# Kernel optimization log

Measured on AMD Instinct MI355X. Metric: run time of the kernel, lower is better.

The kernel has to match this reference:

```python
import jax, jax.numpy as jnp
import numpy as np
import math

T = 120      # frame_num == audio_len == max_seq_len
D = 64       # hidden_layer_size
H = 2        # n_head
DH = D // H
DFF = 2 * D
DOUT = 31
PERIOD = 10
EPS = 1e-5
NEG = -1e9
SCALE = 1.0 / math.sqrt(DH)
SLOPES = (1.0 / 16.0, 1.0 / 256.0)  # ALiBi slopes for n_head=2


def _pe():
    # PeriodicPositionalEncoding: sinusoid over one period, tiled
    pos = jnp.arange(PERIOD, dtype=jnp.float32)[:, None]
    div = jnp.exp(jnp.arange(0, D, 2, dtype=jnp.float32) * (-math.log(10000.0) / D))
    s, c = jnp.sin(pos * div), jnp.cos(pos * div)
    pe = jnp.stack([s, c], axis=-1).reshape(PERIOD, D)  # interleave sin/cos
    return jnp.tile(pe, (T // PERIOD + 1, 1))[:T]


def _alibi_mask():
    # causal mask + ALiBi bias: alibi[i,j] = -slope * floor((i-j)/period) for j<=i
    slopes = jnp.array(SLOPES, dtype=jnp.float32)
    i = jnp.arange(T)[:, None]
    j = jnp.arange(T)[None, :]
    rel = ((i - j) // PERIOD).astype(jnp.float32)
    return jnp.where(j <= i, -slopes[:, None, None] * rel, NEG)  # [H,T,T]


def _ln(x, g, b):
    m = x.mean(-1, keepdims=True)
    v = ((x - m) ** 2).mean(-1, keepdims=True)
    return (x - m) / jnp.sqrt(v + EPS) * g + b


def setup_inputs() -> dict:
    key = jax.random.key(0)
    ks = iter(jax.random.split(key, 32))
    n = lambda shape, s=0.05: jax.random.normal(next(ks), shape, dtype=jnp.float32) * s
    inp = {
        'audio': jax.random.normal(next(ks), (1, T, 1024), dtype=jnp.float32),
        'W_audio': n((D, 1024)), 'b_audio': n((D,)),
        'obj_W': n((D, 5)),
        'Wq': n((D, D)), 'bq': n((D,)), 'Wk': n((D, D)), 'bk': n((D,)),
        'Wv': n((D, D)), 'bv': n((D,)), 'Wo': n((D, D)), 'bo': n((D,)),
        'Wv2': n((D, D)), 'bv2': n((D,)), 'Wo2': n((D, D)), 'bo2': n((D,)),
        'g1': jnp.ones((D,)), 'be1': jnp.zeros((D,)),
        'g2': jnp.ones((D,)), 'be2': jnp.zeros((D,)),
        'g3': jnp.ones((D,)), 'be3': jnp.zeros((D,)),
        'W1': n((DFF, D)), 'c1': n((DFF,)), 'W2': n((D, DFF)), 'c2': n((D,)),
        'Wr': n((DOUT, D)), 'br': n((DOUT,)), 'Wm': n((D, DOUT)), 'bm': n((D,)),
    }
    return inp


def _forward(audio, W_audio, b_audio, obj_W, Wq, bq, Wk, bk, Wv, bv, Wo, bo,
             Wv2, bv2, Wo2, bo2, g1, be1, g2, be2, g3, be3,
             W1, c1, W2, c2, Wr, br, Wm, bm):
    mem = audio[0] @ W_audio.T + b_audio          # [S,D], S == T
    style = obj_W[:, 0]                            # obj_vector @ [1,0,0,0,0]
    pe = _pe()
    mask = _alibi_mask()
    slopes = jnp.array(SLOPES, dtype=jnp.float32)
    jarr = jnp.arange(T)

    # enc_dec_mask leaves exactly one memory key per target row (anti-diagonal
    # from the end); the feedback row t at step t always attends memory[-1],
    # so its cross-attn output is just the projected value of the last frame.
    cross_last = (mem[-1] @ Wv2.T + bv2) @ Wo2.T + bo2  # [D]

    def step(emb, t):
        # decode only the last row (row t) of the growing sequence; 1-layer
        # post-norm decoder => row t depends only on input rows 0..t.
        x = emb + pe                                 # PPE over prefix
        xq = jnp.take(x, t, axis=0)                  # [D]
        q = (xq @ Wq.T + bq).reshape(H, DH)
        k = (x @ Wk.T + bk).reshape(T, H, DH)
        v = (x @ Wv.T + bv).reshape(T, H, DH)
        bias = jnp.where(jarr <= t,
                         -slopes[:, None] * ((t - jarr) // PERIOD).astype(jnp.float32),
                         NEG)                        # [H,T]
        sc = jnp.einsum('hd,shd->hs', q, k) * SCALE + bias
        a = jax.nn.softmax(sc, axis=-1)
        sa = jnp.einsum('hs,shd->hd', a, v).reshape(D) @ Wo.T + bo
        h1 = _ln(xq + sa, g1, be1)
        h2 = _ln(h1 + cross_last, g2, be2)
        h3 = _ln(h2 + jax.nn.relu(h2 @ W1.T + c1) @ W2.T + c2, g3, be3)
        new = (h3 @ Wr.T + br) @ Wm.T + bm + style   # vertice_map(vertice_map_r(.)) + style
        emb = jax.lax.dynamic_update_slice(emb, new[None, :], (t + 1, 0))
        return emb, None

    emb0 = jnp.zeros((T, D), audio.dtype).at[0].set(style)
    emb, _ = jax.lax.scan(step, emb0, jnp.arange(T - 1))

    # final full-length decode (last loop iteration of the torch module)
    x = emb + pe
    q = (x @ Wq.T + bq).reshape(T, H, DH)
    k = (x @ Wk.T + bk).reshape(T, H, DH)
    v = (x @ Wv.T + bv).reshape(T, H, DH)
    sc = jnp.einsum('thd,shd->hts', q, k) * SCALE + mask
    a = jax.nn.softmax(sc, axis=-1)
    sa = jnp.einsum('hts,shd->thd', a, v).reshape(T, D) @ Wo.T + bo
    h1 = _ln(x + sa, g1, be1)
    # at length T with S == T the enc_dec_mask aligns target row j <-> memory row j
    cross = (mem @ Wv2.T + bv2) @ Wo2.T + bo2
    h2 = _ln(h1 + cross, g2, be2)
    h3 = _ln(h2 + jax.nn.relu(h2 @ W1.T + c1) @ W2.T + c2, g3, be3)
    return (h3 @ Wr.T + br)[None]                    # [1,T,31]


def reference(audio, W_audio, b_audio, obj_W, Wq, bq, Wk, bk, Wv, bv, Wo, bo,
              Wv2, bv2, Wo2, bo2, g1, be1, g2, be2, g3, be3,
              W1, c1, W2, c2, Wr, br, Wm, bm):
    return _forward(audio, W_audio, b_audio, obj_W, Wq, bq, Wk, bk, Wv, bv, Wo, bo,
                    Wv2, bv2, Wo2, bo2, g1, be1, g2, be2, g3, be3,
                    W1, c1, W2, c2, Wr, br, Wm, bm)
```

## Files before the change

kernel.cpp:

```cpp
#include <hip/hip_runtime.h>

typedef unsigned short u16;
typedef unsigned int   u32;
typedef _Float16 f16;
typedef f16 h2 __attribute__((ext_vector_type(2)));
typedef f16 h4 __attribute__((ext_vector_type(4)));
typedef f16 h8 __attribute__((ext_vector_type(8)));

#define T_    120
#define D_    64
#define DOUT_ 31
#define KROW_ 68
#define VROW_ 132

#if defined(__has_builtin)
#if __has_builtin(__builtin_amdgcn_fdot2)
#define DOT2(a,b,c) __builtin_amdgcn_fdot2((a),(b),(c),false)
#endif
#endif
#ifndef DOT2
#define DOT2(a,b,c) ((float)(a).x*(float)(b).x + ((float)(a).y*(float)(b).y + (c)))
#endif
#define SHV(x,i,j) __builtin_shufflevector((x),(x),(i),(j))

__device__ __forceinline__ h2 pk(float a, float b){
#if defined(__has_builtin) && __has_builtin(__builtin_amdgcn_cvt_pkrtz)
  return __builtin_bit_cast(h2, __builtin_amdgcn_cvt_pkrtz(a, b));
#else
  h2 r; r.x = (f16)a; r.y = (f16)b; return r;
#endif
}
__device__ __forceinline__ float b2f(u16 u){ return __uint_as_float(((u32)u) << 16); }
__device__ __forceinline__ float2 bp2(u32 u){
  float2 r; r.x = __uint_as_float(u << 16); r.y = __uint_as_float(u & 0xffff0000u); return r;
}
__device__ __forceinline__ u16 f2bu(float f){
  u32 u = __float_as_uint(f);
  u32 r = u + 0x7fffu + ((u >> 16) & 1u);
  return (u16)(r >> 16);
}
__device__ __forceinline__ u16 f2h16(float x){
  f16 v = (f16)x; u16 r; __builtin_memcpy(&r, &v, 2); return r;
}
#define WSYNC() do{ __asm__ __volatile__("" ::: "memory"); __builtin_amdgcn_wave_barrier(); }while(0)

__device__ __forceinline__ float dpp_sum(float x){
  int t;
  t = __builtin_amdgcn_update_dpp(0, __float_as_int(x), 0x111, 0xf, 0xf, true); x += __int_as_float(t);
  t = __builtin_amdgcn_update_dpp(0, __float_as_int(x), 0x112, 0xf, 0xf, true); x += __int_as_float(t);
  t = __builtin_amdgcn_update_dpp(0, __float_as_int(x), 0x114, 0xf, 0xf, true); x += __int_as_float(t);
  t = __builtin_amdgcn_update_dpp(0, __float_as_int(x), 0x118, 0xf, 0xf, true); x += __int_as_float(t);
  t = __builtin_amdgcn_update_dpp(0, __float_as_int(x), 0x142, 0xf, 0xf, true); x += __int_as_float(t);
  t = __builtin_amdgcn_update_dpp(0, __float_as_int(x), 0x143, 0xf, 0xf, true); x += __int_as_float(t);
  return __int_as_float(__builtin_amdgcn_readlane(__float_as_int(x), 63));
}
__device__ __forceinline__ float dpp_max_pos(float x){
  int t;
  t = __builtin_amdgcn_update_dpp(0, __float_as_int(x), 0x111, 0xf, 0xf, true); x = fmaxf(x, __int_as_float(t));
  t = __builtin_amdgcn_update_dpp(0, __float_as_int(x), 0x112, 0xf, 0xf, true); x = fmaxf(x, __int_as_float(t));
  t = __builtin_amdgcn_update_dpp(0, __float_as_int(x), 0x114, 0xf, 0xf, true); x = fmaxf(x, __int_as_float(t));
  t = __builtin_amdgcn_update_dpp(0, __float_as_int(x), 0x118, 0xf, 0xf, true); x = fmaxf(x, __int_as_float(t));
  t = __builtin_amdgcn_update_dpp(0, __float_as_int(x), 0x142, 0xf, 0xf, true); x = fmaxf(x, __int_as_float(t));
  t = __builtin_amdgcn_update_dpp(0, __float_as_int(x), 0x143, 0xf, 0xf, true); x = fmaxf(x, __int_as_float(t));
  return __int_as_float(__builtin_amdgcn_readlane(__float_as_int(x), 63));
}
__device__ __forceinline__ float pe_val(int row, int i){
  const float coef = -0.28782313662425574f;
  int p = row % 10;
  float dv  = __expf((float)(i >> 1) * coef);
  float ang = (float)p * dv;
  return (i & 1) ? __cosf(ang) : __sinf(ang);
}
__device__ __forceinline__ void loadrow32(h2* dst, const float* row){
  #pragma unroll
  for (int r = 0; r < 16; ++r){
    float4 f = ((const float4*)row)[r];
    dst[2*r]   = pk(f.x, f.y);
    dst[2*r+1] = pk(f.z, f.w);
  }
}

__global__ __launch_bounds__(256) void k_pre(const float* __restrict__ audio,
                                             const float* __restrict__ Wa, const float* __restrict__ ba,
                                             const float* __restrict__ Wv2, const float* __restrict__ bv2,
                                             const float* __restrict__ Wo2, const float* __restrict__ bo2,
                                             const float* __restrict__ Wo, const float* __restrict__ W1,
                                             const float* __restrict__ W2, const float* __restrict__ Wr,
                                             const float* __restrict__ Wm, const float* __restrict__ br,
                                             const float* __restrict__ bm,
                                             float* __restrict__ cross, float* __restrict__ Ms,
                                             float* __restrict__ bMv,
                                             u16* __restrict__ wob, u16* __restrict__ w1b,
                                             u16* __restrict__ w2b, u16* __restrict__ wrb){
  const int b = blockIdx.x, tid = threadIdx.x;
  if (b == 120){
    for (int i = tid; i < 4096; i += 256) wob[i] = f2bu(Wo[i]);
    for (int i = tid; i < 8192; i += 256){ w1b[i] = f2bu(W1[i]); w2b[i] = f2bu(W2[i]); }
    for (int i = tid; i < 1984; i += 256) wrb[i] = f2bu(Wr[i]);
    for (int idx = tid; idx < 4096; idx += 256){
      int d = idx >> 6, e = idx & 63;
      float acc = 0.f;
      #pragma unroll
      for (int j = 0; j < 31; ++j) acc += Wm[d*31 + j] * Wr[j*64 + e];
      Ms[idx] = acc;
    }
    if (tid < 64){
      float acc = bm[tid];
      #pragma unroll
      for (int j = 0; j < 31; ++j) acc += Wm[tid*31 + j] * br[j];
      bMv[tid] = acc;
    }
    return;
  }
  __shared__ float ash[1024];
  __shared__ float msh[64], tsh[64];
  for (int i = tid; i < 1024; i += 256) ash[i] = audio[b*1024 + i];
  __syncthreads();
  const int w = tid >> 6, lane = tid & 63;
  for (int d = w*16; d < w*16 + 16; ++d){
    const float4* row = (const float4*)(Wa + d*1024);
    float acc = 0.f;
    #pragma unroll
    for (int m = 0; m < 4; ++m){
      float4 wp = row[lane + 64*m];
      int j = 4*(lane + 64*m);
      acc += wp.x*ash[j] + wp.y*ash[j+1] + wp.z*ash[j+2] + wp.w*ash[j+3];
    }
    acc = dpp_sum(acc);
    if (lane == 0) msh[d] = acc + ba[d];
  }
  __syncthreads();
  if (tid < 64){
    const float4* r1 = (const float4*)(Wv2 + tid*64);
    float a = bv2[tid];
    #pragma unroll
    for (int j = 0; j < 16; ++j){ float4 p = r1[j]; a += p.x*msh[4*j] + p.y*msh[4*j+1] + p.z*msh[4*j+2] + p.w*msh[4*j+3]; }
    tsh[tid] = a;
  }
  __syncthreads();
  if (tid < 64){
    const float4* r2 = (const float4*)(Wo2 + tid*64);
    float c = bo2[tid];
    #pragma unroll
    for (int j = 0; j < 16; ++j){ float4 p = r2[j]; c += p.x*tsh[4*j] + p.y*tsh[4*j+1] + p.z*tsh[4*j+2] + p.w*tsh[4*j+3]; }
    cross[b*64 + tid] = c;
  }
}

__global__ __launch_bounds__(128, 1) void k_scan(
    const float* __restrict__ objW,
    const float* __restrict__ Wq, const float* __restrict__ bq,
    const float* __restrict__ Wk, const float* __restrict__ bk,
    const float* __restrict__ Wv, const float* __restrict__ bv,
    const float* __restrict__ Wo, const float* __restrict__ bo,
    const float* __restrict__ g1, const float* __restrict__ be1,
    const float* __restrict__ g2, const float* __restrict__ be2,
    const float* __restrict__ g3, const float* __restrict__ be3,
    const float* __restrict__ W1, const float* __restrict__ c1,
    const float* __restrict__ W2, const float* __restrict__ c2,
    const float* __restrict__ Ms, const float* __restrict__ bMv,
    const float* __restrict__ cross,
    u16* __restrict__ xw16, u16* __restrict__ Kw16, u16* __restrict__ Vw16)
{
  __shared__ __align__(16) f16 KcS[128*KROW_];
  __shared__ __align__(16) f16 VcS[D_*VROW_];
  __shared__ __align__(16) f16 xwS[T_*D_];
  __shared__ __align__(16) f16 sch[256];
  __shared__ __align__(16) f16 xh[64], qh[64], ath[64], h2h[64], h3h[64];
  __shared__ __align__(16) f16 fsh[128];
  __shared__ float at_p1[64], h2f[64], xf[64];
  __shared__ float pe_tab[640];

  const int tid = threadIdx.x;
  const int i = tid & 63;
  const bool w0 = tid < 64;

  h2 A[32], B[32], C[32], D[32], E[32];
  float biasA=0.f, biasB=0.f, bo_r=0.f, c1r=0.f, c2_r=0.f, bmst=0.f, cls_r=0.f;
  float g1r=0.f,b1r=0.f,g2r=0.f,b2r=0.f,g3r=0.f,b3r=0.f;

  if (w0){
    loadrow32(A, Wq + i*64);
    loadrow32(B, Wv + i*64);
    loadrow32(C, Wo + i*64);
    loadrow32(D, W1 + i*64);
    biasA = bq[i]; biasB = bv[i]; bo_r = bo[i]; c1r = c1[i];
    g1r = g1[i]; b1r = be1[i]; g2r = g2[i]; b2r = be2[i];
    cls_r = cross[119*64 + i];
  } else {
    loadrow32(A, Wk + i*64);
    loadrow32(B, W1 + (64+i)*64);
    loadrow32(C, W2 + i*128);
    loadrow32(D, W2 + i*128 + 64);
    loadrow32(E, Ms + i*64);
    biasA = bk[i]; c1r = c1[64+i]; c2_r = c2[i];
    g3r = g3[i]; b3r = be3[i];
    bmst = bMv[i] + objW[i*5];
  }
  { u32* p = (u32*)KcS; for (int idx = tid; idx < 128*KROW_/2; idx += 128) p[idx] = 0; }
  { u32* p = (u32*)VcS; for (int idx = tid; idx < D_*VROW_/2;  idx += 128) p[idx] = 0; }
  for (int idx = tid; idx < 640; idx += 128) pe_tab[idx] = pe_val(idx >> 6, idx & 63);
  if (w0){
    float st = objW[i*5];
    float x0 = st + pe_val(0, i);
    xf[i] = x0; xh[i] = (f16)x0; xwS[i] = (f16)x0;
  }
  __syncthreads();

  int pp = 1;
  for (int t = 0; t < T_-1; ++t){
    {
      const h8* xv = (const h8*)xh;
      if (w0){
        float q0=biasA,q1=0.f,q2=0.f,q3=0.f, v0=biasB,v1=0.f,v2=0.f,v3=0.f;
        #pragma unroll
        for (int r = 0; r < 8; ++r){
          h8 x = xv[r];
          h2 xa=SHV(x,0,1), xb=SHV(x,2,3), xc=SHV(x,4,5), xd=SHV(x,6,7);
          q0 = DOT2(A[4*r+0], xa, q0); q1 = DOT2(A[4*r+1], xb, q1);
          q2 = DOT2(A[4*r+2], xc, q2); q3 = DOT2(A[4*r+3], xd, q3);
          v0 = DOT2(B[4*r+0], xa, v0); v1 = DOT2(B[4*r+1], xb, v1);
          v2 = DOT2(B[4*r+2], xc, v2); v3 = DOT2(B[4*r+3], xd, v3);
        }
        qh[i] = (f16)((q0+q1)+(q2+q3));
        VcS[i*VROW_ + t] = (f16)((v0+v1)+(v2+v3));
      } else {
        float k0=biasA,k1=0.f,k2=0.f,k3=0.f;
        #pragma unroll
        for (int r = 0; r < 8; ++r){
          h8 x = xv[r];
          k0 = DOT2(A[4*r+0], SHV(x,0,1), k0);
          k1 = DOT2(A[4*r+1], SHV(x,2,3), k1);
          k2 = DOT2(A[4*r+2], SHV(x,4,5), k2);
          k3 = DOT2(A[4*r+3], SHV(x,6,7), k3);
        }
        KcS[t*KROW_ + i] = (f16)((k0+k1)+(k2+k3));
      }
    }
    __syncthreads();
    {
      const int h = tid >> 6, j = i;
      const h8* qv = (const h8*)(qh + h*32);
      const h4* k0 = (const h4*)(KcS + j*KROW_ + h*32);
      const h4* k1 = (const h4*)(KcS + (j+64)*KROW_ + h*32);
      float d0a=0.f,d0b=0.f,d1a=0.f,d1b=0.f;
      #pragma unroll
      for (int r = 0; r < 4; ++r){
        h8 q = qv[r];
        h4 ka = k0[2*r], kb = k0[2*r+1], kc = k1[2*r], kd = k1[2*r+1];
        d0a = DOT2(SHV(ka,0,1), SHV(q,0,1), d0a);
        d0b = DOT2(SHV(ka,2,3), SHV(q,2,3), d0b);
        d0a = DOT2(SHV(kb,0,1), SHV(q,4,5), d0a);
        d0b = DOT2(SHV(kb,2,3), SHV(q,6,7), d0b);
        d1a = DOT2(SHV(kc,0,1), SHV(q,0,1), d1a);
        d1b = DOT2(SHV(kc,2,3), SHV(q,2,3), d1b);
        d1a = DOT2(SHV(kd,0,1), SHV(q,4,5), d1a);
        d1b = DOT2(SHV(kd,2,3), SHV(q,6,7), d1b);
      }
      float d0 = d0a + d0b, d1 = d1a + d1b;
      const float slope = h ? 0.00390625f : 0.0625f;
      int r0 = (t - j) / 10, r1 = (t - j - 64) / 10;
      float s0 = (j      <= t) ? d0*0.17677669529663687f - slope*(float)r0 : -1e30f;
      float s1 = (j + 64 <= t) ? d1*0.17677669529663687f - slope*(float)r1 : -1e30f;
      float m = dpp_max_pos(fmaxf(s0, s1) + 16384.f) - 16384.f;
      float e0 = (j      <= t) ? __expf(s0 - m) : 0.f;
      float e1 = (j + 64 <= t) ? __expf(s1 - m) : 0.f;
      float inv = 1.f / dpp_sum(e0 + e1);
      sch[h*128 + j]      = (f16)(e0*inv);
      sch[h*128 + j + 64] = (f16)(e1*inv);
    }
    __syncthreads();
    float atp0 = 0.f;
    {
      const int hd = i >> 5;
      const h8* av = (const h8*)(sch + hd*128) + (w0 ? 0 : 8);
      const h4* vv = (const h4*)(VcS + i*VROW_) + (w0 ? 0 : 16);
      float p0=0.f,p1=0.f,p2=0.f,p3=0.f;
      #pragma unroll
      for (int r = 0; r < 8; ++r){
        h8 a = av[r];
        h4 va = vv[2*r], vb = vv[2*r+1];
        p0 = DOT2(SHV(va,0,1), SHV(a,0,1), p0);
        p1 = DOT2(SHV(va,2,3), SHV(a,2,3), p1);
        p2 = DOT2(SHV(vb,0,1), SHV(a,4,5), p2);
        p3 = DOT2(SHV(vb,2,3), SHV(a,6,7), p3);
      }
      float p = (p0+p1)+(p2+p3);
      if (!w0) at_p1[i] = p; else atp0 = p;
    }
    __syncthreads();
    if (w0){
      float atv = atp0 + at_p1[i];
      ath[i] = (f16)atv;
      WSYNC();
      const h8* av = (const h8*)ath;
      float a0=bo_r, a1=0.f, a2=0.f, a3=0.f;
      #pragma unroll
      for (int r = 0; r < 8; ++r){
        h8 x = av[r];
        a0 = DOT2(C[4*r+0], SHV(x,0,1), a0);
        a1 = DOT2(C[4*r+1], SHV(x,2,3), a1);
        a2 = DOT2(C[4*r+2], SHV(x,4,5), a2);
        a3 = DOT2(C[4*r+3], SHV(x,6,7), a3);
      }
      float y = xf[i] + (a0+a1)+(a2+a3);
      float s = dpp_sum(y), s2 = dpp_sum(y*y);
      float m = s*(1.f/64.f), var = fmaxf(s2*(1.f/64.f) - m*m, 0.f);
      float h1 = (y - m)*rsqrtf(var + 1e-5f)*g1r + b1r;
      float z = h1 + cls_r;
      float sz = dpp_sum(z), sz2 = dpp_sum(z*z);
      float mz = sz*(1.f/64.f), vz = fmaxf(sz2*(1.f/64.f) - mz*mz, 0.f);
      float h2v = (z - mz)*rsqrtf(vz + 1e-5f)*g2r + b2r;
      h2h[i] = (f16)h2v;
      h2f[i] = h2v;
    }
    __syncthreads();
    {
      const h8* hv = (const h8*)h2h;
      float a0=c1r, a1=0.f, a2=0.f, a3=0.f;
      if (w0){
        #pragma unroll
        for (int r = 0; r < 8; ++r){
          h8 x = hv[r];
          a0 = DOT2(D[4*r+0], SHV(x,0,1), a0);
          a1 = DOT2(D[4*r+1], SHV(x,2,3), a1);
          a2 = DOT2(D[4*r+2], SHV(x,4,5), a2);
          a3 = DOT2(D[4*r+3], SHV(x,6,7), a3);
        }
      } else {
        #pragma unroll
        for (int r = 0; r < 8; ++r){
          h8 x = hv[r];
          a0 = DOT2(B[4*r+0], SHV(x,0,1), a0);
          a1 = DOT2(B[4*r+1], SHV(x,2,3), a1);
          a2 = DOT2(B[4*r+2], SHV(x,4,5), a2);
          a3 = DOT2(B[4*r+3], SHV(x,6,7), a3);
        }
      }
      fsh[tid] = (f16)fmaxf((a0+a1)+(a2+a3), 0.f);
    }
    __syncthreads();
    if (!w0){
      const h8* fv = (const h8*)fsh;
      float a0=c2_r, a1=0.f, a2=0.f, a3=0.f;
      #pragma unroll
      for (int r = 0; r < 8; ++r){
        h8 x = fv[r];
        a0 = DOT2(C[4*r+0], SHV(x,0,1), a0);
        a1 = DOT2(C[4*r+1], SHV(x,2,3), a1);
        a2 = DOT2(C[4*r+2], SHV(x,4,5), a2);
        a3 = DOT2(C[4*r+3], SHV(x,6,7), a3);
      }
      #pragma unroll
      for (int r = 0; r < 8; ++r){
        h8 x = fv[8+r];
        a0 = DOT2(D[4*r+0], SHV(x,0,1), a0);
        a1 = DOT2(D[4*r+1], SHV(x,2,3), a1);
        a2 = DOT2(D[4*r+2], SHV(x,4,5), a2);
        a3 = DOT2(D[4*r+3], SHV(x,6,7), a3);
      }
      float y = h2f[i] + (a0+a1)+(a2+a3);
      float s = dpp_sum(y), s2 = dpp_sum(y*y);
      float m = s*(1.f/64.f), var = fmaxf(s2*(1.f/64.f) - m*m, 0.f);
      float h3v = (y - m)*rsqrtf(var + 1e-5f)*g3r + b3r;
      h3h[i] = (f16)h3v;
      WSYNC();
      const h8* hv3 = (const h8*)h3h;
      float m0=bmst, m1=0.f, m2=0.f, m3=0.f;
      #pragma unroll
      for (int r = 0; r < 8; ++r){
        h8 x = hv3[r];
        m0 = DOT2(E[4*r+0], SHV(x,0,1), m0);
        m1 = DOT2(E[4*r+1], SHV(x,2,3), m1);
        m2 = DOT2(E[4*r+2], SHV(x,4,5), m2);
        m3 = DOT2(E[4*r+3], SHV(x,6,7), m3);
      }
      float xn = (m0+m1)+(m2+m3) + pe_tab[pp*64 + i];
      xf[i] = xn;
      xh[i] = (f16)xn;
      xwS[(t+1)*64 + i] = (f16)xn;
    }
    __syncthreads();
    pp = (pp == 9) ? 0 : pp + 1;
  }
  {
    const h8* xv = (const h8*)xh;
    if (w0){
      float v0=biasB,v1=0.f,v2=0.f,v3=0.f;
      #pragma unroll
      for (int r = 0; r < 8; ++r){
        h8 x = xv[r];
        v0 = DOT2(B[4*r+0], SHV(x,0,1), v0);
        v1 = DOT2(B[4*r+1], SHV(x,2,3), v1);
        v2 = DOT2(B[4*r+2], SHV(x,4,5), v2);
        v3 = DOT2(B[4*r+3], SHV(x,6,7), v3);
      }
      Vw16[119*64 + i] = f2h16((v0+v1)+(v2+v3));
    } else {
      float k0=biasA,k1=0.f,k2=0.f,k3=0.f;
      #pragma unroll
      for (int r = 0; r < 8; ++r){
        h8 x = xv[r];
        k0 = DOT2(A[4*r+0], SHV(x,0,1), k0);
        k1 = DOT2(A[4*r+1], SHV(x,2,3), k1);
        k2 = DOT2(A[4*r+2], SHV(x,4,5), k2);
        k3 = DOT2(A[4*r+3], SHV(x,6,7), k3);
      }
      Kw16[119*64 + i] = f2h16((k0+k1)+(k2+k3));
    }
  }
  {
    const u16* kc = (const u16*)KcS;
    const u16* vc = (const u16*)VcS;
    for (int idx = tid; idx < 119*64; idx += 128){
      int t_ = idx >> 6, d = idx & 63;
      Kw16[idx] = kc[t_*KROW_ + d];
      Vw16[idx] = vc[d*VROW_ + t_];
    }
    const u32* xs32 = (const u32*)xwS;
    for (int idx = tid; idx < T_*D_/2; idx += 128) ((u32*)xw16)[idx] = xs32[idx];
  }
}

__global__ __launch_bounds__(128) void k_final(
    const float* __restrict__ Wq, const float* __restrict__ bq, const float* __restrict__ bo,
    const float* __restrict__ g1, const float* __restrict__ be1,
    const float* __restrict__ g2, const float* __restrict__ be2,
    const float* __restrict__ g3, const float* __restrict__ be3,
    const float* __restrict__ c1, const float* __restrict__ c2, const float* __restrict__ br,
    const u16* __restrict__ wo_b, const u16* __restrict__ w1_b,
    const u16* __restrict__ w2_b, const u16* __restrict__ wr_b,
    const float* __restrict__ cross, const u16* __restrict__ xw16,
    const u16* __restrict__ Kw16, const u16* __restrict__ Vw16,
    float* __restrict__ out)
{
  __shared__ float xs[64], qs[64], at[64], h2s[64], h3s[64], fs[128], sc[256];
  const int irow = blockIdx.x, tid = threadIdx.x;
  const f16* xp = (const f16*)xw16;
  const f16* kp = (const f16*)Kw16;
  const f16* vp = (const f16*)Vw16;
  if (tid < 64) xs[tid] = (float)xp[irow*64 + tid];
  __syncthreads();
  if (tid < 64){
    const float4* wr_ = (const float4*)(Wq + tid*64);
    float acc = bq[tid];
    #pragma unroll
    for (int j = 0; j < 16; ++j){ float4 w = wr_[j]; acc += w.x*xs[4*j] + w.y*xs[4*j+1] + w.z*xs[4*j+2] + w.w*xs[4*j+3]; }
    qs[tid] = acc;
  }
  __syncthreads();
  {
    const int h = tid >> 6, j = tid & 63;
    const float* qh_ = qs + h*32;
    float d0 = 0.f, d1 = 0.f;
    const h4* k0 = (const h4*)(kp + j*64 + h*32);
    #pragma unroll
    for (int w = 0; w < 8; ++w){
      h4 p = k0[w];
      d0 += (float)p.x*qh_[4*w] + (float)p.y*qh_[4*w+1] + (float)p.z*qh_[4*w+2] + (float)p.w*qh_[4*w+3];
    }
    if (j < 56){
      const h4* k1 = (const h4*)(kp + (j+64)*64 + h*32);
      #pragma unroll
      for (int w = 0; w < 8; ++w){
        h4 p = k1[w];
        d1 += (float)p.x*qh_[4*w] + (float)p.y*qh_[4*w+1] + (float)p.z*qh_[4*w+2] + (float)p.w*qh_[4*w+3];
      }
    }
    const float slope = h ? 0.00390625f : 0.0625f;
    float s0 = (j      <= irow) ? d0*0.17677669529663687f - slope*(float)((irow-j)/10)    : -1e30f;
    float s1 = (j + 64 <= irow) ? d1*0.17677669529663687f - slope*(float)((irow-j-64)/10) : -1e30f;
    float m = dpp_max_pos(fmaxf(s0, s1) + 16384.f) - 16384.f;
    float e0 = (j      <= irow) ? __expf(s0 - m) : 0.f;
    float e1 = (j + 64 <= irow) ? __expf(s1 - m) : 0.f;
    float inv = 1.f / dpp_sum(e0 + e1);
    sc[h*128 + j]      = e0*inv;
    sc[h*128 + j + 64] = e1*inv;
  }
  __syncthreads();
  if (tid < 64){
    const float* a = sc + (tid >> 5)*128;
    float a0=0.f,a1=0.f,a2=0.f,a3=0.f;
    #pragma unroll
    for (int jj = 0; jj < 30; ++jj){
      a0 += a[4*jj]   * (float)vp[(4*jj)*64   + tid];
      a1 += a[4*jj+1] * (float)vp[(4*jj+1)*64 + tid];
      a2 += a[4*jj+2] * (float)vp[(4*jj+2)*64 + tid];
      a3 += a[4*jj+3] * (float)vp[(4*jj+3)*64 + tid];
    }
    at[tid] = (a0+a1)+(a2+a3);
  }
  __syncthreads();
  if (tid < 64){
    const u32* orow = (const u32*)(wo_b + tid*64);
    float acc = bo[tid];
    #pragma unroll
    for (int w = 0; w < 32; ++w){ float2 p = bp2(orow[w]); acc += p.x*at[2*w] + p.y*at[2*w+1]; }
    float y = xs[tid] + acc;
    float s = dpp_sum(y), s2 = dpp_sum(y*y);
    float m = s*(1.f/64.f), var = fmaxf(s2*(1.f/64.f) - m*m, 0.f);
    float h1 = (y - m)*rsqrtf(var + 1e-5f)*g1[tid] + be1[tid];
    float z = h1 + cross[irow*64 + tid];
    float sz = dpp_sum(z), sz2 = dpp_sum(z*z);
    float mz = sz*(1.f/64.f), vz = fmaxf(sz2*(1.f/64.f) - mz*mz, 0.f);
    h2s[tid] = (z - mz)*rsqrtf(vz + 1e-5f)*g2[tid] + be2[tid];
  }
  __syncthreads();
  {
    const u32* w1r = (const u32*)(w1_b + tid*64);
    float acc = c1[tid];
    #pragma unroll
    for (int w = 0; w < 32; ++w){ float2 p = bp2(w1r[w]); acc += p.x*h2s[2*w] + p.y*h2s[2*w+1]; }
    fs[tid] = fmaxf(acc, 0.f);
  }
  __syncthreads();
  if (tid < 64){
    const u32* w2r = (const u32*)(w2_b + tid*128);
    float acc = c2[tid];
    #pragma unroll
    for (int w = 0; w < 64; ++w){ float2 p = bp2(w2r[w]); acc += p.x*fs[2*w] + p.y*fs[2*w+1]; }
    float y = h2s[tid] + acc;
    float s = dpp_sum(y), s2 = dpp_sum(y*y);
    float m = s*(1.f/64.f), var = fmaxf(s2*(1.f/64.f) - m*m, 0.f);
    h3s[tid] = (y - m)*rsqrtf(var + 1e-5f)*g3[tid] + be3[tid];
  }
  __syncthreads();
  if (tid < DOUT_){
    const u32* rr = (const u32*)(wr_b + tid*64);
    float acc = br[tid];
    #pragma unroll
    for (int w = 0; w < 32; ++w){ float2 p = bp2(rr[w]); acc += p.x*h3s[2*w] + p.y*h3s[2*w+1]; }
    out[irow*DOUT_ + tid] = acc;
  }
}

extern "C" void kernel_launch(void* const* d_in, const int* in_sizes, int n_in,
                              void* d_out, int out_size, void* d_ws, size_t ws_size,
                              hipStream_t stream){
  const float* audio=(const float*)d_in[0];
  const float* Wa   =(const float*)d_in[1];
  const float* ba   =(const float*)d_in[2];
  const float* objW =(const float*)d_in[3];
  const float* Wq   =(const float*)d_in[4];
  const float* bq   =(const float*)d_in[5];
  const float* Wk   =(const float*)d_in[6];
  const float* bk   =(const float*)d_in[7];
  const float* Wv   =(const float*)d_in[8];
  const float* bv   =(const float*)d_in[9];
  const float* Wo   =(const float*)d_in[10];
  const float* bo   =(const float*)d_in[11];
  const float* Wv2  =(const float*)d_in[12];
  const float* bv2  =(const float*)d_in[13];
  const float* Wo2  =(const float*)d_in[14];
  const float* bo2  =(const float*)d_in[15];
  const float* g1   =(const float*)d_in[16];
  const float* be1  =(const float*)d_in[17];
  const float* g2   =(const float*)d_in[18];
  const float* be2  =(const float*)d_in[19];
  const float* g3   =(const float*)d_in[20];
  const float* be3  =(const float*)d_in[21];
  const float* W1   =(const float*)d_in[22];
  const float* c1   =(const float*)d_in[23];
  const float* W2   =(const float*)d_in[24];
  const float* c2   =(const float*)d_in[25];
  const float* Wr   =(const float*)d_in[26];
  const float* br   =(const float*)d_in[27];
  const float* Wm   =(const float*)d_in[28];
  const float* bm   =(const float*)d_in[29];

  float* ws    = (float*)d_ws;
  float* cross = ws;
  float* Ms    = ws + 7680;
  float* bMv   = ws + 11776;
  u16* xw16 = (u16*)(ws + 11840);
  u16* Kw16 = xw16 + 7680;
  u16* Vw16 = Kw16 + 7680;
  u16* wo_b = Vw16 + 7680;
  u16* w1_b = wo_b + 4096;
  u16* w2_b = w1_b + 8192;
  u16* wr_b = w2_b + 8192;
  float* out = (float*)d_out;

  k_pre  <<<dim3(121), dim3(256), 0, stream>>>(audio, Wa, ba, Wv2, bv2, Wo2, bo2,
                                               Wo, W1, W2, Wr, Wm, br, bm,
                                               cross, Ms, bMv, wo_b, w1_b, w2_b, wr_b);
  k_scan <<<dim3(1),   dim3(128), 0, stream>>>(objW, Wq, bq, Wk, bk, Wv, bv, Wo, bo,
                                               g1, be1, g2, be2, g3, be3,
                                               W1, c1, W2, c2, Ms, bMv,
                                               cross, xw16, Kw16, Vw16);
  k_final<<<dim3(120), dim3(128), 0, stream>>>(Wq, bq, bo, g1, be1, g2, be2, g3, be3,
                                               c1, c2, br, wo_b, w1_b, w2_b, wr_b,
                                               cross, xw16, Kw16, Vw16, out);
}
```

Before: 393.7 us.

## Defer softmax normalization, fold LN3 into motion projection, rebalance QKV work

The attention softmax drops the max-reduction and instead clamps exponents, applying the 1/sum normalization after the AV and Wo products, so the reduction overlaps with the AV work. LayerNorm3's gain and bias are folded into the Ms projection weights so the LN statistics reduction runs alongside the dot products. The V projection moves after the first barrier so Q/K and V are computed in parallel across both waves, and the second-half AV product is skipped while t<64. Clamping exponents at 8 and skipping the max subtraction risk fp16 overflow or precision drift.

```diff
diff --git a/kernel.cpp b/kernel.cpp
--- a/kernel.cpp
+++ b/kernel.cpp
@@ -41,6 +41,13 @@
 }
 __device__ __forceinline__ u16 f2h16(float x){
   f16 v = (f16)x; u16 r; __builtin_memcpy(&r, &v, 2); return r;
+}
+__device__ __forceinline__ float fast_rcp(float x){
+#if defined(__has_builtin) && __has_builtin(__builtin_amdgcn_rcpf)
+  return __builtin_amdgcn_rcpf(x);
+#else
+  return 1.f / x;
+#endif
 }
 #define WSYNC() do{ __asm__ __volatile__("" ::: "memory"); __builtin_amdgcn_wave_barrier(); }while(0)
 
@@ -166,9 +173,11 @@
   __shared__ __align__(16) f16 VcS[D_*VROW_];
   __shared__ __align__(16) f16 xwS[T_*D_];
   __shared__ __align__(16) f16 sch[256];
-  __shared__ __align__(16) f16 xh[64], qh[64], ath[64], h2h[64], h3h[64];
+  __shared__ __align__(16) f16 xh[64], qh[64], h2h[64], h3h[64];
+  __shared__ __align__(16) f16 at0h[64], at1h[64];
   __shared__ __align__(16) f16 fsh[128];
-  __shared__ float at_p1[64], h2f[64], xf[64];
+  __shared__ float h2f[64], xf[64];
+  __shared__ float invSh;
   __shared__ float pe_tab[640];
 
   const int tid = threadIdx.x;
@@ -176,8 +185,9 @@
   const bool w0 = tid < 64;
 
   h2 A[32], B[32], C[32], D[32], E[32];
-  float biasA=0.f, biasB=0.f, bo_r=0.f, c1r=0.f, c2_r=0.f, bmst=0.f, cls_r=0.f;
-  float g1r=0.f,b1r=0.f,g2r=0.f,b2r=0.f,g3r=0.f,b3r=0.f;
+  float biasA=0.f, biasB=0.f, bo_r=0.f, c1r=0.f, c2_r=0.f, cls_r=0.f;
+  float g1r=0.f,b1r=0.f,g2r=0.f,b2r=0.f;
+  float mg_r=0.f, u_r=0.f;
 
   if (w0){
     loadrow32(A, Wq + i*64);
@@ -192,10 +202,24 @@
     loadrow32(B, W1 + (64+i)*64);
     loadrow32(C, W2 + i*128);
     loadrow32(D, W2 + i*128 + 64);
-    loadrow32(E, Ms + i*64);
+    {
+      const float4* mr  = (const float4*)(Ms + i*64);
+      const float4* gv  = (const float4*)g3;
+      const float4* b3v = (const float4*)be3;
+      float mg = 0.f, mb = 0.f;
+      #pragma unroll
+      for (int r = 0; r < 16; ++r){
+        float4 f = mr[r], g = gv[r], b = b3v[r];
+        float e0 = f.x*g.x, e1 = f.y*g.y, e2 = f.z*g.z, e3 = f.w*g.w;
+        E[2*r]   = pk(e0, e1);
+        E[2*r+1] = pk(e2, e3);
+        mg += (e0+e1)+(e2+e3);
+        mb += f.x*b.x + f.y*b.y + f.z*b.z + f.w*b.w;
+      }
+      mg_r = mg;
+      u_r  = bMv[i] + objW[i*5] + mb;
+    }
     biasA = bk[i]; c1r = c1[64+i]; c2_r = c2[i];
-    g3r = g3[i]; b3r = be3[i];
-    bmst = bMv[i] + objW[i*5];
   }
   { u32* p = (u32*)KcS; for (int idx = tid; idx < 128*KROW_/2; idx += 128) p[idx] = 0; }
   { u32* p = (u32*)VcS; for (int idx = tid; idx < D_*VROW_/2;  idx += 128) p[idx] = 0; }
@@ -209,36 +233,36 @@
 
   int pp = 1;
   for (int t = 0; t < T_-1; ++t){
+    float e0r, e1r, inv0v;
+    h8 xr[8];
     {
       const h8* xv = (const h8*)xh;
-      if (w0){
-        float q0=biasA,q1=0.f,q2=0.f,q3=0.f, v0=biasB,v1=0.f,v2=0.f,v3=0.f;
-        #pragma unroll
-        for (int r = 0; r < 8; ++r){
-          h8 x = xv[r];
-          h2 xa=SHV(x,0,1), xb=SHV(x,2,3), xc=SHV(x,4,5), xd=SHV(x,6,7);
-          q0 = DOT2(A[4*r+0], xa, q0); q1 = DOT2(A[4*r+1], xb, q1);
-          q2 = DOT2(A[4*r+2], xc, q2); q3 = DOT2(A[4*r+3], xd, q3);
-          v0 = DOT2(B[4*r+0], xa, v0); v1 = DOT2(B[4*r+1], xb, v1);
-          v2 = DOT2(B[4*r+2], xc, v2); v3 = DOT2(B[4*r+3], xd, v3);
-        }
-        qh[i] = (f16)((q0+q1)+(q2+q3));
-        VcS[i*VROW_ + t] = (f16)((v0+v1)+(v2+v3));
-      } else {
-        float k0=biasA,k1=0.f,k2=0.f,k3=0.f;
-        #pragma unroll
-        for (int r = 0; r < 8; ++r){
-          h8 x = xv[r];
-          k0 = DOT2(A[4*r+0], SHV(x,0,1), k0);
-          k1 = DOT2(A[4*r+1], SHV(x,2,3), k1);
-          k2 = DOT2(A[4*r+2], SHV(x,4,5), k2);
-          k3 = DOT2(A[4*r+3], SHV(x,6,7), k3);
-        }
-        KcS[t*KROW_ + i] = (f16)((k0+k1)+(k2+k3));
-      }
+      #pragma unroll
+      for (int r = 0; r < 8; ++r) xr[r] = xv[r];
+      float a0=biasA,a1=0.f,a2=0.f,a3=0.f;
+      #pragma unroll
+      for (int r = 0; r < 8; ++r){
+        h8 x = xr[r];
+        a0 = DOT2(A[4*r+0], SHV(x,0,1), a0);
+        a1 = DOT2(A[4*r+1], SHV(x,2,3), a1);
+        a2 = DOT2(A[4*r+2], SHV(x,4,5), a2);
+        a3 = DOT2(A[4*r+3], SHV(x,6,7), a3);
+      }
+      float qk = (a0+a1)+(a2+a3);
+      if (w0) qh[i] = (f16)qk; else KcS[t*KROW_ + i] = (f16)qk;
     }
     __syncthreads();
     {
+      if (w0){
+        float v0=biasB,v1=0.f,v2=0.f,v3=0.f;
+        #pragma unroll
+        for (int r = 0; r < 8; ++r){
+          h8 x = xr[r];
+          v0 = DOT2(B[4*r+0], SHV(x,0,1), v0); v1 = DOT2(B[4*r+1], SHV(x,2,3), v1);
+          v2 = DOT2(B[4*r+2], SHV(x,4,5), v2); v3 = DOT2(B[4*r+3], SHV(x,6,7), v3);
+        }
+        VcS[i*VROW_ + t] = (f16)((v0+v1)+(v2+v3));
+      }
       const int h = tid >> 6, j = i;
       const h8* qv = (const h8*)(qh + h*32);
       const h4* k0 = (const h4*)(KcS + j*KROW_ + h*32);
@@ -260,50 +284,74 @@
       float d0 = d0a + d0b, d1 = d1a + d1b;
       const float slope = h ? 0.00390625f : 0.0625f;
       int r0 = (t - j) / 10, r1 = (t - j - 64) / 10;
-      float s0 = (j      <= t) ? d0*0.17677669529663687f - slope*(float)r0 : -1e30f;
-      float s1 = (j + 64 <= t) ? d1*0.17677669529663687f - slope*(float)r1 : -1e30f;
-      float m = dpp_max_pos(fmaxf(s0, s1) + 16384.f) - 16384.f;
-      float e0 = (j      <= t) ? __expf(s0 - m) : 0.f;
-      float e1 = (j + 64 <= t) ? __expf(s1 - m) : 0.f;
-      float inv = 1.f / dpp_sum(e0 + e1);
-      sch[h*128 + j]      = (f16)(e0*inv);
-      sch[h*128 + j + 64] = (f16)(e1*inv);
+      float s0 = d0*0.17677669529663687f - slope*(float)r0;
+      float s1 = d1*0.17677669529663687f - slope*(float)r1;
+      e0r = (j      <= t) ? __expf(fminf(s0, 8.f)) : 0.f;
+      e1r = (j + 64 <= t) ? __expf(fminf(s1, 8.f)) : 0.f;
+      sch[h*128 + j]      = (f16)e0r;
+      sch[h*128 + j + 64] = (f16)e1r;
     }
     __syncthreads();
-    float atp0 = 0.f;
     {
-      const int hd = i >> 5;
-      const h8* av = (const h8*)(sch + hd*128) + (w0 ? 0 : 8);
-      const h4* vv = (const h4*)(VcS + i*VROW_) + (w0 ? 0 : 16);
-      float p0=0.f,p1=0.f,p2=0.f,p3=0.f;
-      #pragma unroll
-      for (int r = 0; r < 8; ++r){
-        h8 a = av[r];
-        h4 va = vv[2*r], vb = vv[2*r+1];
-        p0 = DOT2(SHV(va,0,1), SHV(a,0,1), p0);
-        p1 = DOT2(SHV(va,2,3), SHV(a,2,3), p1);
-        p2 = DOT2(SHV(vb,0,1), SHV(a,4,5), p2);
-        p3 = DOT2(SHV(vb,2,3), SHV(a,6,7), p3);
-      }
-      float p = (p0+p1)+(p2+p3);
-      if (!w0) at_p1[i] = p; else atp0 = p;
+      float den = dpp_sum(e0r + e1r);
+      float inv = fast_rcp(den);
+      inv0v = inv;
+      if (tid == 64) invSh = inv;
+      if (w0 || t >= 64){
+        const int hd = i >> 5;
+        const h8* av = (const h8*)(sch + hd*128) + (w0 ? 0 : 8);
+        const h4* vv = (const h4*)(VcS + i*VROW_) + (w0 ? 0 : 16);
+        float p0=0.f,p1=0.f,p2=0.f,p3=0.f;
+        #pragma unroll
+        for (int r = 0; r < 8; ++r){
+          h8 a = av[r];
+          h4 va = vv[2*r], vb = vv[2*r+1];
+          p0 = DOT2(SHV(va,0,1), SHV(a,0,1), p0);
+          p1 = DOT2(SHV(va,2,3), SHV(a,2,3), p1);
+          p2 = DOT2(SHV(vb,0,1), SHV(a,4,5), p2);
+          p3 = DOT2(SHV(vb,2,3), SHV(a,6,7), p3);
+        }
+        float p = (p0+p1)+(p2+p3);
+        if (w0) at0h[i] = (f16)p; else at1h[i] = (f16)p;
+      }
     }
     __syncthreads();
     if (w0){
-      float atv = atp0 + at_p1[i];
-      ath[i] = (f16)atv;
-      WSYNC();
-      const h8* av = (const h8*)ath;
-      float a0=bo_r, a1=0.f, a2=0.f, a3=0.f;
-      #pragma unroll
-      for (int r = 0; r < 8; ++r){
-        h8 x = av[r];
-        a0 = DOT2(C[4*r+0], SHV(x,0,1), a0);
-        a1 = DOT2(C[4*r+1], SHV(x,2,3), a1);
-        a2 = DOT2(C[4*r+2], SHV(x,4,5), a2);
-        a3 = DOT2(C[4*r+3], SHV(x,6,7), a3);
-      }
-      float y = xf[i] + (a0+a1)+(a2+a3);
+      float inv1v = invSh;
+      float xfv = xf[i];
+      float l0=0.f,l1=0.f,hh0=0.f,hh1=0.f;
+      {
+        const h8* a0v = (const h8*)at0h;
+        #pragma unroll
+        for (int r = 0; r < 4; ++r){
+          h8 x = a0v[r];
+          l0 = DOT2(C[4*r+0], SHV(x,0,1), l0); l1 = DOT2(C[4*r+1], SHV(x,2,3), l1);
+          l0 = DOT2(C[4*r+2], SHV(x,4,5), l0); l1 = DOT2(C[4*r+3], SHV(x,6,7), l1);
+        }
+        #pragma unroll
+        for (int r = 4; r < 8; ++r){
+          h8 x = a0v[r];
+          hh0 = DOT2(C[4*r+0], SHV(x,0,1), hh0); hh1 = DOT2(C[4*r+1], SHV(x,2,3), hh1);
+          hh0 = DOT2(C[4*r+2], SHV(x,4,5), hh0); hh1 = DOT2(C[4*r+3], SHV(x,6,7), hh1);
+        }
+      }
+      if (t >= 64){
+        const h8* a1v = (const h8*)at1h;
+        #pragma unroll
+        for (int r = 0; r < 4; ++r){
+          h8 x = a1v[r];
+          l0 = DOT2(C[4*r+0], SHV(x,0,1), l0); l1 = DOT2(C[4*r+1], SHV(x,2,3), l1);
+          l0 = DOT2(C[4*r+2], SHV(x,4,5), l0); l1 = DOT2(C[4*r+3], SHV(x,6,7), l1);
+        }
+        #pragma unroll
+        for (int r = 4; r < 8; ++r){
+          h8 x = a1v[r];
+          hh0 = DOT2(C[4*r+0], SHV(x,0,1), hh0); hh1 = DOT2(C[4*r+1], SHV(x,2,3), hh1);
+          hh0 = DOT2(C[4*r+2], SHV(x,4,5), hh0); hh1 = DOT2(C[4*r+3], SHV(x,6,7), hh1);
+        }
+      }
+      float sa = bo_r + inv0v*(l0+l1) + inv1v*(hh0+hh1);
+      float y = xfv + sa;
       float s = dpp_sum(y), s2 = dpp_sum(y*y);
       float m = s*(1.f/64.f), var = fmaxf(s2*(1.f/64.f) - m*m, 0.f);
       float h1 = (y - m)*rsqrtf(var + 1e-5f)*g1r + b1r;
@@ -341,6 +389,8 @@
     }
     __syncthreads();
     if (!w0){
+      float pe_c  = pe_tab[pp*64 + i];
+      float h2v_s = h2f[i];
       const h8* fv = (const h8*)fsh;
       float a0=c2_r, a1=0.f, a2=0.f, a3=0.f;
       #pragma unroll
@@ -359,23 +409,26 @@
         a2 = DOT2(D[4*r+2], SHV(x,4,5), a2);
         a3 = DOT2(D[4*r+3], SHV(x,6,7), a3);
       }
-      float y = h2f[i] + (a0+a1)+(a2+a3);
-      float s = dpp_sum(y), s2 = dpp_sum(y*y);
-      float m = s*(1.f/64.f), var = fmaxf(s2*(1.f/64.f) - m*m, 0.f);
-      float h3v = (y - m)*rsqrtf(var + 1e-5f)*g3r + b3r;
-      h3h[i] = (f16)h3v;
+      float y3 = h2v_s + (a0+a1)+(a2+a3);
+      h3h[i] = (f16)y3;
       WSYNC();
       const h8* hv3 = (const h8*)h3h;
-      float m0=bmst, m1=0.f, m2=0.f, m3=0.f;
+      h8 yr[8];
+      #pragma unroll
+      for (int r = 0; r < 8; ++r) yr[r] = hv3[r];
+      float s = dpp_sum(y3), s2 = dpp_sum(y3*y3);
+      float m = s*(1.f/64.f), var = fmaxf(s2*(1.f/64.f) - m*m, 0.f);
+      float invs = rsqrtf(var + 1e-5f);
+      float m0=0.f, m1=0.f, m2=0.f, m3=0.f;
       #pragma unroll
       for (int r = 0; r < 8; ++r){
-        h8 x = hv3[r];
+        h8 x = yr[r];
         m0 = DOT2(E[4*r+0], SHV(x,0,1), m0);
         m1 = DOT2(E[4*r+1], SHV(x,2,3), m1);
         m2 = DOT2(E[4*r+2], SHV(x,4,5), m2);
         m3 = DOT2(E[4*r+3], SHV(x,6,7), m3);
       }
-      float xn = (m0+m1)+(m2+m3) + pe_tab[pp*64 + i];
+      float xn = ((m0+m1)+(m2+m3))*invs + (u_r - m*invs*mg_r) + pe_c;
       xf[i] = xn;
       xh[i] = (f16)xn;
       xwS[(t+1)*64 + i] = (f16)xn;
```

Measured after the change: 376.2 us. 1.05x faster.
